# Kernel tuning notes

Hardware: AMD Instinct MI355X
Metric: run time of the kernel (lower is better)

The kernel has to match this reference:

```python
import jax, jax.numpy as jnp
import numpy as np

H, W = 8192, 16384          # dna_shape = (out_features, in_features)
NUM_TRANSFORMS = 8
NUM_POINTS = 1000           # hardcoded in source
CHAOS_ITERS = 10            # hardcoded in source
B = 2048


def setup_inputs() -> dict:
    key = jax.random.key(0)
    k1, k2, k3 = jax.random.split(key, 3)
    x = jax.random.normal(k1, (B, W), dtype=jnp.float32)
    # flat IFS params: [a,b,c,d,e,f,p] per transform; scaled down so affine maps are mostly contractive
    dna_params = jax.random.normal(k2, (NUM_TRANSFORMS * 7,), dtype=jnp.float32) * 0.5
    bias = jax.random.normal(k3, (H,), dtype=jnp.float32)
    return {"x": x, "dna_params": dna_params, "bias": bias}


def reference(x, dna_params, bias):
    params = dna_params.reshape(NUM_TRANSFORMS, 7)  # (T, 7)
    # theta[t] = [[a, b, e], [c, d, f]]  -> (T, 2, 3) affine maps
    theta = jnp.stack([
        jnp.stack([params[:, 0], params[:, 1], params[:, 4]], axis=1),
        jnp.stack([params[:, 2], params[:, 3], params[:, 5]], axis=1),
    ], axis=1)

    key = jax.random.key(1)
    kp, kg = jax.random.split(key)
    points = jax.random.uniform(kp, (NUM_POINTS, 2), dtype=x.dtype) * 2.0 - 1.0  # (N, 2) in [-1, 1)
    logits = jnp.broadcast_to(params[:, 6], (NUM_POINTS, NUM_TRANSFORMS))

    # Chaos game: 10 iterations of hard gumbel-softmax transform selection + affine map
    for i in range(CHAOS_ITERS):
        g = jax.random.gumbel(jax.random.fold_in(kg, i), (NUM_POINTS, NUM_TRANSFORMS), dtype=x.dtype)
        soft = jax.nn.softmax(logits + g, axis=-1)  # tau = 1.0
        hard = jax.nn.one_hot(jnp.argmax(soft, axis=-1), NUM_TRANSFORMS, dtype=soft.dtype)
        gw = hard + soft - jax.lax.stop_gradient(soft)          # straight-through hard sample (N, T)
        t_theta = jnp.einsum('nt,trc->nrc', gw, theta)          # (N, 2, 3) per-point affine
        ph = jnp.concatenate([points, jnp.ones((NUM_POINTS, 1), dtype=points.dtype)], axis=1)  # (N, 3)
        points = jnp.einsum('nrc,nc->nr', t_theta, ph)          # (N, 2)

    # Map attractor points to matrix coordinates
    y_coords = (points[:, 1] + 1.0) * 0.5 * (H - 1)
    x_coords = (points[:, 0] + 1.0) * 0.5 * (W - 1)
    y_low = jnp.clip(jnp.floor(y_coords).astype(jnp.int32), 0, H - 2)
    y_w = y_coords - y_low.astype(y_coords.dtype)
    x_low = jnp.clip(jnp.floor(x_coords).astype(jnp.int32), 0, W - 2)
    x_w = x_coords - x_low.astype(x_coords.dtype)

    # Bilinear gather along in_features: (B, N)
    x_vals = x[:, x_low] * (1.0 - x_w) + x[:, x_low + 1] * x_w

    # Bilinear scatter-add along out_features: (B, H)
    y = jnp.zeros((x.shape[0], H), dtype=x.dtype)
    y = y.at[:, y_low].add(x_vals * (1.0 - y_w))
    y = y.at[:, y_low + 1].add(x_vals * y_w)
    return y / NUM_POINTS + bias
```

## Files before the change

kernel.cpp:

```cpp
#include <hip/hip_runtime.h>
#include <stdint.h>

#ifndef PRNG_PARTITIONABLE
#define PRNG_PARTITIONABLE 1
#endif

namespace {

constexpr int kH  = 8192;
constexpr int kW  = 16384;
constexpr int kNT = 8;
constexpr int kNP = 1000;
constexpr int kCI = 10;

typedef float floatx4 __attribute__((ext_vector_type(4)));

__device__ __forceinline__ uint32_t rotl32(uint32_t x, int n) {
  return (x << n) | (x >> (32 - n));
}

__device__ void threefry2x32(uint32_t k0, uint32_t k1, uint32_t c0, uint32_t c1,
                             uint32_t& o0, uint32_t& o1) {
  const uint32_t ks2 = k0 ^ k1 ^ 0x1BD11BDAu;
  uint32_t x0 = c0 + k0, x1 = c1 + k1;
#define TF_R(r) { x0 += x1; x1 = rotl32(x1, (r)); x1 ^= x0; }
  TF_R(13) TF_R(15) TF_R(26) TF_R(6)
  x0 += k1;  x1 += ks2 + 1u;
  TF_R(17) TF_R(29) TF_R(16) TF_R(24)
  x0 += ks2; x1 += k0 + 2u;
  TF_R(13) TF_R(15) TF_R(26) TF_R(6)
  x0 += k0;  x1 += k1 + 3u;
  TF_R(17) TF_R(29) TF_R(16) TF_R(24)
  x0 += k1;  x1 += ks2 + 4u;
  TF_R(13) TF_R(15) TF_R(26) TF_R(6)
  x0 += ks2; x1 += k0 + 5u;
#undef TF_R
  o0 = x0; o1 = x1;
}

__device__ __forceinline__ uint32_t random_bits32(uint32_t k0, uint32_t k1,
                                                  uint32_t i, uint32_t size) {
#if PRNG_PARTITIONABLE
  uint32_t o0, o1;
  threefry2x32(k0, k1, 0u , i, o0, o1);
  (void)size;
  return o0 ^ o1;
#else
  const uint32_t half = size / 2u;
  const uint32_t j = (i < half) ? i : (i - half);
  uint32_t o0, o1;
  threefry2x32(k0, k1, j, j + half, o0, o1);
  return (i < half) ? o0 : o1;
#endif
}

__device__ __forceinline__ float u01(uint32_t bits) {
  return __uint_as_float((bits >> 9) | 0x3f800000u) - 1.0f;
}

__device__ __forceinline__ int cvt_f32_i32_x86(float v) {
  if (!(v >= -2147483648.0f && v < 2147483648.0f)) return (int)0x80000000;
  return (int)v;
}

__global__ __launch_bounds__(256) void fractal_chaos(
    const float* __restrict__ dna, int4* __restrict__ rec) {
  const int gid  = blockIdx.x * blockDim.x + threadIdx.x;
  const int n    = gid >> 3;
  const int lane = gid & 7;
  if (n >= kNP) return;

  uint32_t kp0, kp1, kg0, kg1;
#if PRNG_PARTITIONABLE
  threefry2x32(0u, 1u, 0u, 0u, kp0, kp1);
  threefry2x32(0u, 1u, 0u, 1u, kg0, kg1);
#else
  uint32_t a0, a1, b0, b1;
  threefry2x32(0u, 1u, 0u, 2u, a0, a1);
  threefry2x32(0u, 1u, 1u, 3u, b0, b1);
  kp0 = a0; kp1 = b0; kg0 = a1; kg1 = b1;
#endif

  const float A  = dna[lane * 7 + 0], Bb = dna[lane * 7 + 1];
  const float C  = dna[lane * 7 + 2], D  = dna[lane * 7 + 3];
  const float E  = dna[lane * 7 + 4], F  = dna[lane * 7 + 5];
  const float P  = dna[lane * 7 + 6];

  float z[kCI];
  #pragma unroll
  for (int i = 0; i < kCI; ++i) {
    uint32_t ki0, ki1;
    threefry2x32(kg0, kg1, 0u, (uint32_t)i, ki0, ki1);
    const uint32_t bb = random_bits32(ki0, ki1, (uint32_t)(n * kNT + lane),
                                      (uint32_t)(kNP * kNT));
    const float u = fmaxf(u01(bb), 1.17549435e-38f);
    const float g = -logf(-logf(u));
    z[i] = P + g;
  }

  const uint32_t bx = random_bits32(kp0, kp1, (uint32_t)(2 * n),     2u * kNP);
  const uint32_t by = random_bits32(kp0, kp1, (uint32_t)(2 * n + 1), 2u * kNP);
  float px = u01(bx) * 2.0f - 1.0f;
  float py = u01(by) * 2.0f - 1.0f;

  #pragma unroll
  for (int i = 0; i < kCI; ++i) {
    float zb = z[i];
    int   bt = lane;
    #pragma unroll
    for (int m = 1; m < 8; m <<= 1) {
      const float zo = __shfl_xor(zb, m, 8);
      const int   to = __shfl_xor(bt, m, 8);
      if (zo > zb || (zo == zb && to < bt)) { zb = zo; bt = to; }
    }
    const float A_ = __shfl(A,  bt, 8), B_ = __shfl(Bb, bt, 8);
    const float C_ = __shfl(C,  bt, 8), D_ = __shfl(D,  bt, 8);
    const float E_ = __shfl(E,  bt, 8), F_ = __shfl(F,  bt, 8);
    const float nx = A_ * px + B_ * py + E_;
    const float ny = C_ * px + D_ * py + F_;
    px = nx; py = ny;
  }

  if (lane == 0) {
    const float xc = ((px + 1.0f) * 0.5f) * (float)(kW - 1);
    const float yc = ((py + 1.0f) * 0.5f) * (float)(kH - 1);
    int xl = cvt_f32_i32_x86(floorf(xc));
    int yl = cvt_f32_i32_x86(floorf(yc));
    xl = min(max(xl, 0), kW - 2);
    yl = min(max(yl, 0), kH - 2);
    const float xw = xc - (float)xl;
    const float yw = yc - (float)yl;
    rec[n] = make_int4(xl, __float_as_int(xw), yl, __float_as_int(yw));
  }
}

__global__ __launch_bounds__(1024) void fractal_apply(
    const float* __restrict__ x, const float* __restrict__ bias,
    const int4* __restrict__ rec, float* __restrict__ out) {
  __shared__ __align__(16) float acc[kH];
  __shared__ __align__(16) float xbuf[kW / 2];

  const int b   = blockIdx.x;
  const int tid = threadIdx.x;

  float4* acc4 = reinterpret_cast<float4*>(acc);
  acc4[tid]        = make_float4(0.f, 0.f, 0.f, 0.f);
  acc4[tid + 1024] = make_float4(0.f, 0.f, 0.f, 0.f);

  const bool havept = tid < kNP;
  int xl = 0, yl = 0;
  float xw = 0.f, yw = 0.f, xw0 = 0.f, w0 = 0.f;
  if (havept) {
    const int4 r = rec[tid];
    xl = r.x; xw = __int_as_float(r.y);
    yl = r.z; yw = __int_as_float(r.w);
    xw0 = 1.0f - xw; w0 = 1.0f - yw;
  }

  const float* __restrict__ xrow = x + (size_t)b * kW;
  float4* xbuf4 = reinterpret_cast<float4*>(xbuf);

  #pragma unroll
  for (int p = 0; p < 2; ++p) {
    const float4* __restrict__ src =
        reinterpret_cast<const float4*>(xrow + p * (kW / 2));
    xbuf4[tid]        = src[tid];
    xbuf4[tid + 1024] = src[tid + 1024];
    __syncthreads();

    if (havept && (xl >> 13) == p) {
      const int loc = xl & (kW / 2 - 1);
      const float v0 = xbuf[loc];
      const float v1 = (loc < kW / 2 - 1) ? xbuf[loc + 1] : xrow[xl + 1];
      const float xv = v0 * xw0 + v1 * xw;
      atomicAdd(&acc[yl],     xv * w0);
      atomicAdd(&acc[yl + 1], xv * yw);
    }
    __syncthreads();
  }

  const float4* __restrict__ bias4 = reinterpret_cast<const float4*>(bias);
  floatx4* __restrict__ out4 =
      reinterpret_cast<floatx4*>(out + (size_t)b * kH);
  #pragma unroll
  for (int i = 0; i < 2; ++i) {
    const int idx = tid + i * 1024;
    const float4 a  = acc4[idx];
    const float4 bi = bias4[idx];
    floatx4 o;
    o.x = a.x / 1000.0f + bi.x;
    o.y = a.y / 1000.0f + bi.y;
    o.z = a.z / 1000.0f + bi.z;
    o.w = a.w / 1000.0f + bi.w;
    __builtin_nontemporal_store(o, &out4[idx]);
  }
}

}

extern "C" void kernel_launch(void* const* d_in, const int* in_sizes, int n_in,
                              void* d_out, int out_size, void* d_ws, size_t ws_size,
                              hipStream_t stream) {
  const float* x    = (const float*)d_in[0];
  const float* dna  = (const float*)d_in[1];
  const float* bias = (const float*)d_in[2];
  float* out = (float*)d_out;
  int4* rec = (int4*)d_ws;

  const int chaosThreads = kNP * 8;
  fractal_chaos<<<(chaosThreads + 255) / 256, 256, 0, stream>>>(dna, rec);

  const int B = in_sizes[0] / kW;
  fractal_apply<<<B, 1024, 0, stream>>>(x, bias, rec, out);
}
```

Before: 50.52 us.

## Replace per-row shared-memory scatter with precomputed CSR gather over output rows

Adds a single-block build kernel that turns the 1000 attractor points into a CSR structure keyed by output row, with pre-scaled weights, an x-sorted point order, and a list of heavily populated rows. The apply kernel no longer stages the whole x row and an 8192-float accumulator in LDS. It gathers only the 1000 needed x values, then computes each output element as a gather-sum over its CSR entries, using wave-level reductions for heavy rows. This removes the large LDS traffic, shared atomics and the 1024-thread blocks. In exchange it adds an extra serial launch and rowptr/entry reads per output element, plus divergence in rows with many entries.

```diff
diff --git a/kernel.cpp b/kernel.cpp
--- a/kernel.cpp
+++ b/kernel.cpp
@@ -12,6 +12,14 @@
 constexpr int kNT = 8;
 constexpr int kNP = 1000;
 constexpr int kCI = 10;
+constexpr int kHeavy = 128;
+constexpr int kMaxHeavy = 32;
+
+constexpr size_t kOffRec    = 0;
+constexpr size_t kOffRowPtr = 16384;
+constexpr size_t kOffEnt    = 49408;
+constexpr size_t kOffOrder  = 65536;
+constexpr size_t kOffHeavy  = 69632;
 
 typedef float floatx4 __attribute__((ext_vector_type(4)));
 
@@ -134,65 +142,178 @@
   }
 }
 
-__global__ __launch_bounds__(1024) void fractal_apply(
+__global__ __launch_bounds__(1024) void fractal_build(
+    const int4* __restrict__ rec, uint32_t* __restrict__ rowptr,
+    uint2* __restrict__ ent, uint32_t* __restrict__ order,
+    uint32_t* __restrict__ heavy ) {
+  __shared__ uint32_t cnt[kH];
+  __shared__ uint32_t seg[1024];
+  __shared__ uint32_t heavyL[kMaxHeavy];
+  __shared__ uint32_t nHeavyL;
+
+  const int t = threadIdx.x;
+  if (t == 0) nHeavyL = 0;
+
+  #pragma unroll
+  for (int i = 0; i < kH / 1024; ++i) cnt[t + i * 1024] = 0;
+  __syncthreads();
+
+  int yl = 0, xl = 0;
+  float w0 = 0.f, w1 = 0.f;
+  const bool hav = t < kNP;
+  if (hav) {
+    const int4 r = rec[t];
+    xl = r.x;
+    yl = r.z;
+    const float yw = __int_as_float(r.w);
+    w0 = (1.0f - yw) * (1.0f / (float)kNP);
+    w1 = yw * (1.0f / (float)kNP);
+    atomicAdd(&cnt[yl], 1u);
+    atomicAdd(&cnt[yl + 1], 1u);
+  }
+  __syncthreads();
+
+  uint32_t s = 0;
+  #pragma unroll
+  for (int i = 0; i < 8; ++i) s += cnt[t * 8 + i];
+  seg[t] = s;
+  __syncthreads();
+  #pragma unroll
+  for (int o = 1; o < 1024; o <<= 1) {
+    uint32_t v = (t >= o) ? seg[t - o] : 0u;
+    __syncthreads();
+    seg[t] += v;
+    __syncthreads();
+  }
+  uint32_t run = (t > 0) ? seg[t - 1] : 0u;
+  const uint32_t total = seg[1023];
+  #pragma unroll
+  for (int i = 0; i < 8; ++i) {
+    const int h = t * 8 + i;
+    const uint32_t c = cnt[h];
+    if (c >= (uint32_t)kHeavy) {
+      const uint32_t p = atomicAdd(&nHeavyL, 1u);
+      if (p < kMaxHeavy) heavyL[p] = (uint32_t)h;
+    }
+    cnt[h] = run;
+    rowptr[h] = run;
+    run += c;
+  }
+  if (t == 1023) rowptr[kH] = total;
+  __syncthreads();
+
+  if (hav) {
+    const uint32_t e0 = atomicAdd(&cnt[yl], 1u);
+    ent[e0] = make_uint2((uint32_t)t, __float_as_uint(w0));
+    const uint32_t e1 = atomicAdd(&cnt[yl + 1], 1u);
+    ent[e1] = make_uint2((uint32_t)t, __float_as_uint(w1));
+  }
+  if (t == 0) heavy[0] = min(nHeavyL, (uint32_t)kMaxHeavy);
+  if (t < kMaxHeavy && t < nHeavyL) heavy[1 + t] = heavyL[t];
+  __syncthreads();
+
+  if (t < 1024) cnt[t] = 0;
+  __syncthreads();
+  const int bx = xl >> 4;
+  if (hav) atomicAdd(&cnt[bx], 1u);
+  __syncthreads();
+  seg[t] = cnt[t];
+  __syncthreads();
+  #pragma unroll
+  for (int o = 1; o < 1024; o <<= 1) {
+    uint32_t v = (t >= o) ? seg[t - o] : 0u;
+    __syncthreads();
+    seg[t] += v;
+    __syncthreads();
+  }
+  cnt[t] = (t > 0) ? seg[t - 1] : 0u;
+  __syncthreads();
+  if (hav) {
+    const uint32_t p = atomicAdd(&cnt[bx], 1u);
+    order[p] = (uint32_t)t;
+  }
+}
+
+__global__ __launch_bounds__(256) void fractal_apply(
     const float* __restrict__ x, const float* __restrict__ bias,
-    const int4* __restrict__ rec, float* __restrict__ out) {
-  __shared__ __align__(16) float acc[kH];
-  __shared__ __align__(16) float xbuf[kW / 2];
-
+    const int4* __restrict__ rec, const uint32_t* __restrict__ rowptr,
+    const uint2* __restrict__ ent, const uint32_t* __restrict__ order,
+    const uint32_t* __restrict__ heavy, float* __restrict__ out) {
+  __shared__ float XV[kNP];
+  __shared__ uint32_t heavyH[kMaxHeavy];
+  __shared__ float heavyS[kMaxHeavy];
+  __shared__ uint32_t nH;
+
+  const int tid = threadIdx.x;
   const int b   = blockIdx.x;
-  const int tid = threadIdx.x;
-
-  float4* acc4 = reinterpret_cast<float4*>(acc);
-  acc4[tid]        = make_float4(0.f, 0.f, 0.f, 0.f);
-  acc4[tid + 1024] = make_float4(0.f, 0.f, 0.f, 0.f);
-
-  const bool havept = tid < kNP;
-  int xl = 0, yl = 0;
-  float xw = 0.f, yw = 0.f, xw0 = 0.f, w0 = 0.f;
-  if (havept) {
-    const int4 r = rec[tid];
-    xl = r.x; xw = __int_as_float(r.y);
-    yl = r.z; yw = __int_as_float(r.w);
-    xw0 = 1.0f - xw; w0 = 1.0f - yw;
-  }
-
   const float* __restrict__ xrow = x + (size_t)b * kW;
-  float4* xbuf4 = reinterpret_cast<float4*>(xbuf);
-
-  #pragma unroll
-  for (int p = 0; p < 2; ++p) {
-    const float4* __restrict__ src =
-        reinterpret_cast<const float4*>(xrow + p * (kW / 2));
-    xbuf4[tid]        = src[tid];
-    xbuf4[tid + 1024] = src[tid + 1024];
-    __syncthreads();
-
-    if (havept && (xl >> 13) == p) {
-      const int loc = xl & (kW / 2 - 1);
-      const float v0 = xbuf[loc];
-      const float v1 = (loc < kW / 2 - 1) ? xbuf[loc + 1] : xrow[xl + 1];
-      const float xv = v0 * xw0 + v1 * xw;
-      atomicAdd(&acc[yl],     xv * w0);
-      atomicAdd(&acc[yl + 1], xv * yw);
-    }
-    __syncthreads();
-  }
-
-  const float4* __restrict__ bias4 = reinterpret_cast<const float4*>(bias);
-  floatx4* __restrict__ out4 =
-      reinterpret_cast<floatx4*>(out + (size_t)b * kH);
-  #pragma unroll
-  for (int i = 0; i < 2; ++i) {
-    const int idx = tid + i * 1024;
-    const float4 a  = acc4[idx];
-    const float4 bi = bias4[idx];
-    floatx4 o;
-    o.x = a.x / 1000.0f + bi.x;
-    o.y = a.y / 1000.0f + bi.y;
-    o.z = a.z / 1000.0f + bi.z;
-    o.w = a.w / 1000.0f + bi.w;
-    __builtin_nontemporal_store(o, &out4[idx]);
+
+  if (tid == 0) nH = heavy[0];
+  if (tid < kMaxHeavy) heavyH[tid] = heavy[1 + tid];
+
+  #pragma unroll
+  for (int j = 0; j < 4; ++j) {
+    const int i = tid + j * 256;
+    if (i < kNP) {
+      const uint32_t n = order[i];
+      const int4 r = rec[n];
+      const int   xl = r.x;
+      const float xw = __int_as_float(r.y);
+      XV[n] = xrow[xl] * (1.0f - xw) + xrow[xl + 1] * xw;
+    }
+  }
+  __syncthreads();
+
+  {
+    const int wid  = tid >> 6;
+    const int lane = tid & 63;
+    const uint32_t nh = nH;
+    for (uint32_t k = wid; k < nh; k += 4) {
+      const uint32_t h = heavyH[k];
+      const uint32_t s = rowptr[h], e = rowptr[h + 1];
+      float p = 0.f;
+      for (uint32_t i = s + lane; i < e; i += 64) {
+        const uint2 en = ent[i];
+        p += XV[en.x] * __uint_as_float(en.y);
+      }
+      #pragma unroll
+      for (int o = 32; o > 0; o >>= 1) p += __shfl_down(p, o);
+      if (lane == 0) heavyS[k] = p;
+    }
+  }
+  __syncthreads();
+
+  const uint32_t nh = nH;
+  const int4* __restrict__ rp4 = reinterpret_cast<const int4*>(rowptr);
+  const floatx4* __restrict__ bias4 = reinterpret_cast<const floatx4*>(bias);
+  floatx4* __restrict__ out4 = reinterpret_cast<floatx4*>(out + (size_t)b * kH);
+
+  #pragma unroll
+  for (int j = 0; j < 8; ++j) {
+    const int g = j * 256 + tid;
+    const int4 rpv = rp4[g];
+    const uint32_t rp_end = rowptr[4 * g + 4];
+    uint32_t rps[5] = {(uint32_t)rpv.x, (uint32_t)rpv.y, (uint32_t)rpv.z,
+                       (uint32_t)rpv.w, rp_end};
+    floatx4 v;
+    #pragma unroll
+    for (int c = 0; c < 4; ++c) {
+      const uint32_t s = rps[c], e = rps[c + 1];
+      float val = 0.f;
+      if (e - s >= (uint32_t)kHeavy) {
+        const uint32_t h = (uint32_t)(4 * g + c);
+        for (uint32_t k = 0; k < nh; ++k)
+          if (heavyH[k] == h) { val = heavyS[k]; break; }
+      } else {
+        for (uint32_t i = s; i < e; ++i) {
+          const uint2 en = ent[i];
+          val += XV[en.x] * __uint_as_float(en.y);
+        }
+      }
+      v[c] = val;
+    }
+    v += bias4[g];
+    __builtin_nontemporal_store(v, &out4[g]);
   }
 }
 
@@ -205,11 +326,18 @@
   const float* dna  = (const float*)d_in[1];
   const float* bias = (const float*)d_in[2];
   float* out = (float*)d_out;
-  int4* rec = (int4*)d_ws;
-
-  const int chaosThreads = kNP * 8;
-  fractal_chaos<<<(chaosThreads + 255) / 256, 256, 0, stream>>>(dna, rec);
+
+  char* ws = (char*)d_ws;
+  int4*     rec    = (int4*)(ws + kOffRec);
+  uint32_t* rowptr = (uint32_t*)(ws + kOffRowPtr);
+  uint2*    ent    = (uint2*)(ws + kOffEnt);
+  uint32_t* order  = (uint32_t*)(ws + kOffOrder);
+  uint32_t* heavy  = (uint32_t*)(ws + kOffHeavy);
+
+  fractal_chaos<<<(kNP * 8 + 255) / 256, 256, 0, stream>>>(dna, rec);
+  fractal_build<<<1, 1024, 0, stream>>>(rec, rowptr, ent, order, heavy);
 
   const int B = in_sizes[0] / kW;
-  fractal_apply<<<B, 1024, 0, stream>>>(x, bias, rec, out);
-}
+  fractal_apply<<<B, 256, 0, stream>>>(x, bias, rec, rowptr, ent, order,
+                                       heavy, out);
+}
```

New measurement: 72.28 us. +43.1%, slower.

## Compact touched output rows and gather x directly instead of staging full rows

Applied to the files above, without the earlier changes.

Adds a single-block build kernel that marks which output columns are hit by the attractor points, builds a bitmap, a prefix-sum compaction of those columns, and per-point compact indices. The apply kernel now reads only the two x values each point needs straight from global memory rather than staging the whole 64 KB row in shared memory. It writes bias directly for untouched columns and accumulates into a small compact shared buffer for touched ones. This cuts global read traffic and shared memory per block, at the cost of an extra serial kernel launch, scattered scalar stores for partially touched vectors, and uncoalesced gathers.

```diff
diff --git a/kernel.cpp b/kernel.cpp
--- a/kernel.cpp
+++ b/kernel.cpp
@@ -12,6 +12,13 @@
 constexpr int kNT = 8;
 constexpr int kNP = 1000;
 constexpr int kCI = 10;
+constexpr int kU  = 2048;
+
+constexpr size_t kOffRec    = 0;
+constexpr size_t kOffRec2   = 16384;
+constexpr size_t kOffBins   = 32768;
+constexpr size_t kOffBitmap = 40960;
+constexpr size_t kOffHdr    = 41984;
 
 typedef float floatx4 __attribute__((ext_vector_type(4)));
 
@@ -134,65 +141,136 @@
   }
 }
 
-__global__ __launch_bounds__(1024) void fractal_apply(
+__global__ __launch_bounds__(1024) void fractal_build(
+    const int4* __restrict__ rec, int4* __restrict__ rec2,
+    uint32_t* __restrict__ bins, uint32_t* __restrict__ bitmap,
+    uint32_t* __restrict__ hdr) {
+  __shared__ uint32_t mark[kH];
+  __shared__ uint32_t seg[1024];
+
+  const int t = threadIdx.x;
+
+  #pragma unroll
+  for (int i = 0; i < kH / 1024; ++i) mark[t + i * 1024] = 0u;
+  __syncthreads();
+
+  int xl = 0, yl = 0;
+  uint32_t xwb = 0, ywb = 0;
+  const bool hav = t < kNP;
+  if (hav) {
+    const int4 r = rec[t];
+    xl = r.x; xwb = (uint32_t)r.y;
+    yl = r.z; ywb = (uint32_t)r.w;
+    mark[yl] = 1u;
+    mark[yl + 1] = 1u;
+  }
+  __syncthreads();
+
+  if (t < kH / 32) {
+    uint32_t w = 0;
+    #pragma unroll
+    for (int j = 0; j < 32; ++j) w |= mark[t * 32 + j] << j;
+    bitmap[t] = w;
+  }
+
+  uint32_t s = 0;
+  #pragma unroll
+  for (int i = 0; i < 8; ++i) s += mark[t * 8 + i];
+  seg[t] = s;
+  __syncthreads();
+  #pragma unroll
+  for (int o = 1; o < 1024; o <<= 1) {
+    uint32_t v = (t >= o) ? seg[t - o] : 0u;
+    __syncthreads();
+    seg[t] += v;
+    __syncthreads();
+  }
+  uint32_t run = (t > 0) ? seg[t - 1] : 0u;
+  if (t == 1023) hdr[0] = seg[1023];
+  #pragma unroll
+  for (int i = 0; i < 8; ++i) {
+    const int h = t * 8 + i;
+    const uint32_t m = mark[h];
+    if (m) bins[run] = (uint32_t)h;
+    mark[h] = run;
+    run += m;
+  }
+  __syncthreads();
+
+  if (hav) {
+    const uint32_t c0 = mark[yl];
+    const uint32_t c1 = mark[yl + 1];
+    rec2[t] = make_int4(xl, (int)xwb, (int)(c0 | (c1 << 16)), (int)ywb);
+  }
+}
+
+__global__ __launch_bounds__(256) void fractal_apply(
     const float* __restrict__ x, const float* __restrict__ bias,
-    const int4* __restrict__ rec, float* __restrict__ out) {
-  __shared__ __align__(16) float acc[kH];
-  __shared__ __align__(16) float xbuf[kW / 2];
-
+    const int4* __restrict__ rec2, const uint32_t* __restrict__ bins,
+    const uint32_t* __restrict__ bitmap, const uint32_t* __restrict__ hdr,
+    float* __restrict__ out) {
+  __shared__ float acc[kU];
+  __shared__ uint32_t bmw[kH / 32];
+
+  const int tid = threadIdx.x;
   const int b   = blockIdx.x;
-  const int tid = threadIdx.x;
+  const float* __restrict__ xrow = x + (size_t)b * kW;
+  float* __restrict__ outrow = out + (size_t)b * kH;
 
   float4* acc4 = reinterpret_cast<float4*>(acc);
-  acc4[tid]        = make_float4(0.f, 0.f, 0.f, 0.f);
-  acc4[tid + 1024] = make_float4(0.f, 0.f, 0.f, 0.f);
-
-  const bool havept = tid < kNP;
-  int xl = 0, yl = 0;
-  float xw = 0.f, yw = 0.f, xw0 = 0.f, w0 = 0.f;
-  if (havept) {
-    const int4 r = rec[tid];
-    xl = r.x; xw = __int_as_float(r.y);
-    yl = r.z; yw = __int_as_float(r.w);
-    xw0 = 1.0f - xw; w0 = 1.0f - yw;
-  }
-
-  const float* __restrict__ xrow = x + (size_t)b * kW;
-  float4* xbuf4 = reinterpret_cast<float4*>(xbuf);
-
-  #pragma unroll
-  for (int p = 0; p < 2; ++p) {
-    const float4* __restrict__ src =
-        reinterpret_cast<const float4*>(xrow + p * (kW / 2));
-    xbuf4[tid]        = src[tid];
-    xbuf4[tid + 1024] = src[tid + 1024];
-    __syncthreads();
-
-    if (havept && (xl >> 13) == p) {
-      const int loc = xl & (kW / 2 - 1);
-      const float v0 = xbuf[loc];
-      const float v1 = (loc < kW / 2 - 1) ? xbuf[loc + 1] : xrow[xl + 1];
-      const float xv = v0 * xw0 + v1 * xw;
-      atomicAdd(&acc[yl],     xv * w0);
-      atomicAdd(&acc[yl + 1], xv * yw);
-    }
-    __syncthreads();
-  }
-
-  const float4* __restrict__ bias4 = reinterpret_cast<const float4*>(bias);
-  floatx4* __restrict__ out4 =
-      reinterpret_cast<floatx4*>(out + (size_t)b * kH);
-  #pragma unroll
-  for (int i = 0; i < 2; ++i) {
-    const int idx = tid + i * 1024;
-    const float4 a  = acc4[idx];
-    const float4 bi = bias4[idx];
-    floatx4 o;
-    o.x = a.x / 1000.0f + bi.x;
-    o.y = a.y / 1000.0f + bi.y;
-    o.z = a.z / 1000.0f + bi.z;
-    o.w = a.w / 1000.0f + bi.w;
-    __builtin_nontemporal_store(o, &out4[idx]);
+  acc4[tid]       = make_float4(0.f, 0.f, 0.f, 0.f);
+  acc4[tid + 256] = make_float4(0.f, 0.f, 0.f, 0.f);
+  bmw[tid] = bitmap[tid];
+  const uint32_t U = hdr[0];
+  __syncthreads();
+
+  int4  r[4];
+  float v0[4], v1[4];
+  #pragma unroll
+  for (int j = 0; j < 4; ++j) {
+    const int n = tid + j * 256;
+    if (n < kNP) {
+      r[j] = rec2[n];
+      v0[j] = xrow[r[j].x];
+      v1[j] = xrow[r[j].x + 1];
+    }
+  }
+
+  const floatx4* __restrict__ bias4 = reinterpret_cast<const floatx4*>(bias);
+  floatx4* __restrict__ outrow4 = reinterpret_cast<floatx4*>(outrow);
+  #pragma unroll
+  for (int j = 0; j < 8; ++j) {
+    const int g = j * 256 + tid;
+    const floatx4 bv = bias4[g];
+    const uint32_t nib = (bmw[g >> 3] >> ((g & 7) * 4)) & 0xFu;
+    if (nib == 0) {
+      __builtin_nontemporal_store(bv, &outrow4[g]);
+    } else {
+      float* o = outrow + 4 * g;
+      if (!(nib & 1u)) o[0] = bv.x;
+      if (!(nib & 2u)) o[1] = bv.y;
+      if (!(nib & 4u)) o[2] = bv.z;
+      if (!(nib & 8u)) o[3] = bv.w;
+    }
+  }
+
+  #pragma unroll
+  for (int j = 0; j < 4; ++j) {
+    const int n = tid + j * 256;
+    if (n < kNP) {
+      const float xw = __int_as_float(r[j].y);
+      const float yw = __int_as_float(r[j].w);
+      const uint32_t c01 = (uint32_t)r[j].z;
+      const float xv = v0[j] * (1.0f - xw) + v1[j] * xw;
+      atomicAdd(&acc[c01 & 0xFFFFu], xv * (1.0f - yw));
+      atomicAdd(&acc[c01 >> 16],     xv * yw);
+    }
+  }
+  __syncthreads();
+
+  for (uint32_t i = tid; i < U; i += 256) {
+    const uint32_t c = bins[i];
+    outrow[c] = acc[i] / 1000.0f + bias[c];
   }
 }
 
@@ -205,11 +283,17 @@
   const float* dna  = (const float*)d_in[1];
   const float* bias = (const float*)d_in[2];
   float* out = (float*)d_out;
-  int4* rec = (int4*)d_ws;
-
-  const int chaosThreads = kNP * 8;
-  fractal_chaos<<<(chaosThreads + 255) / 256, 256, 0, stream>>>(dna, rec);
+
+  char* ws = (char*)d_ws;
+  int4*     rec    = (int4*)(ws + kOffRec);
+  int4*     rec2   = (int4*)(ws + kOffRec2);
+  uint32_t* bins   = (uint32_t*)(ws + kOffBins);
+  uint32_t* bitmap = (uint32_t*)(ws + kOffBitmap);
+  uint32_t* hdr    = (uint32_t*)(ws + kOffHdr);
+
+  fractal_chaos<<<(kNP * 8 + 255) / 256, 256, 0, stream>>>(dna, rec);
+  fractal_build<<<1, 1024, 0, stream>>>(rec, rec2, bins, bitmap, hdr);
 
   const int B = in_sizes[0] / kW;
-  fractal_apply<<<B, 1024, 0, stream>>>(x, bias, rec, out);
-}
+  fractal_apply<<<B, 256, 0, stream>>>(x, bias, rec2, bins, bitmap, hdr, out);
+}
```

New measurement: 80.76 us. +59.8%, slower.

## Gather x values directly per point and process several rows per block

Applied to the files above, without the earlier changes.

Instead of staging each full 64 KB x row through shared memory, each point-thread now loads only its two needed x values straight from global memory, prefetching the next row while the current one is scattered. Each block handles four batch rows, reusing the loaded point records and re-zeroing the LDS accumulator between rows. Barriers become a custom waitcnt-plus-s_barrier sequence. This cuts x read traffic to only the touched elements and reduces block launch and setup overhead. In exchange, global loads become scattered and there are fewer, longer-lived blocks.

```diff
diff --git a/kernel.cpp b/kernel.cpp
--- a/kernel.cpp
+++ b/kernel.cpp
@@ -12,8 +12,11 @@
 constexpr int kNT = 8;
 constexpr int kNP = 1000;
 constexpr int kCI = 10;
+constexpr int kRPB = 4;
 
 typedef float floatx4 __attribute__((ext_vector_type(4)));
+
+#define BAR_LDS() asm volatile("s_waitcnt lgkmcnt(0)\n\ts_barrier" ::: "memory")
 
 __device__ __forceinline__ uint32_t rotl32(uint32_t x, int n) {
   return (x << n) | (x >> (32 - n));
@@ -136,63 +139,75 @@
 
 __global__ __launch_bounds__(1024) void fractal_apply(
     const float* __restrict__ x, const float* __restrict__ bias,
-    const int4* __restrict__ rec, float* __restrict__ out) {
+    const int4* __restrict__ rec, float* __restrict__ out, int B) {
   __shared__ __align__(16) float acc[kH];
-  __shared__ __align__(16) float xbuf[kW / 2];
-
-  const int b   = blockIdx.x;
   const int tid = threadIdx.x;
+  const int r0  = blockIdx.x * kRPB;
+
+  const bool hav = tid < kNP;
+  int xl = 0, yl = 0;
+  float xw = 0.f, yw = 0.f;
+  if (hav) {
+    const int4 rr = rec[tid];
+    xl = rr.x; xw = __int_as_float(rr.y);
+    yl = rr.z; yw = __int_as_float(rr.w);
+  }
+  const float xw0 = 1.0f - xw;
+  const float w0  = 1.0f - yw;
 
   float4* acc4 = reinterpret_cast<float4*>(acc);
   acc4[tid]        = make_float4(0.f, 0.f, 0.f, 0.f);
   acc4[tid + 1024] = make_float4(0.f, 0.f, 0.f, 0.f);
 
-  const bool havept = tid < kNP;
-  int xl = 0, yl = 0;
-  float xw = 0.f, yw = 0.f, xw0 = 0.f, w0 = 0.f;
-  if (havept) {
-    const int4 r = rec[tid];
-    xl = r.x; xw = __int_as_float(r.y);
-    yl = r.z; yw = __int_as_float(r.w);
-    xw0 = 1.0f - xw; w0 = 1.0f - yw;
-  }
-
-  const float* __restrict__ xrow = x + (size_t)b * kW;
-  float4* xbuf4 = reinterpret_cast<float4*>(xbuf);
+  float v0 = 0.f, v1 = 0.f;
+  if (hav && r0 < B) {
+    const float* xp = x + (size_t)r0 * kW + xl;
+    v0 = xp[0];
+    v1 = xp[1];
+  }
+
+  BAR_LDS();
+
+  const floatx4* __restrict__ bias4 = reinterpret_cast<const floatx4*>(bias);
 
   #pragma unroll
-  for (int p = 0; p < 2; ++p) {
-    const float4* __restrict__ src =
-        reinterpret_cast<const float4*>(xrow + p * (kW / 2));
-    xbuf4[tid]        = src[tid];
-    xbuf4[tid + 1024] = src[tid + 1024];
-    __syncthreads();
-
-    if (havept && (xl >> 13) == p) {
-      const int loc = xl & (kW / 2 - 1);
-      const float v0 = xbuf[loc];
-      const float v1 = (loc < kW / 2 - 1) ? xbuf[loc + 1] : xrow[xl + 1];
+  for (int it = 0; it < kRPB; ++it) {
+    const int r = r0 + it;
+    if (r >= B) break;
+
+    if (hav) {
       const float xv = v0 * xw0 + v1 * xw;
       atomicAdd(&acc[yl],     xv * w0);
       atomicAdd(&acc[yl + 1], xv * yw);
     }
-    __syncthreads();
-  }
-
-  const float4* __restrict__ bias4 = reinterpret_cast<const float4*>(bias);
-  floatx4* __restrict__ out4 =
-      reinterpret_cast<floatx4*>(out + (size_t)b * kH);
-  #pragma unroll
-  for (int i = 0; i < 2; ++i) {
-    const int idx = tid + i * 1024;
-    const float4 a  = acc4[idx];
-    const float4 bi = bias4[idx];
-    floatx4 o;
-    o.x = a.x / 1000.0f + bi.x;
-    o.y = a.y / 1000.0f + bi.y;
-    o.z = a.z / 1000.0f + bi.z;
-    o.w = a.w / 1000.0f + bi.w;
-    __builtin_nontemporal_store(o, &out4[idx]);
+
+    if (hav && it + 1 < kRPB && r + 1 < B) {
+      const float* xp = x + (size_t)(r + 1) * kW + xl;
+      v0 = xp[0];
+      v1 = xp[1];
+    }
+
+    BAR_LDS();
+
+    float* __restrict__ outrow = out + (size_t)r * kH;
+    floatx4* __restrict__ out4 = reinterpret_cast<floatx4*>(outrow);
+    #pragma unroll
+    for (int j = 0; j < 2; ++j) {
+      const int g = tid + j * 1024;
+      const float4 a  = acc4[g];
+      const floatx4 bi = bias4[g];
+      floatx4 o;
+      o.x = a.x / 1000.0f + bi.x;
+      o.y = a.y / 1000.0f + bi.y;
+      o.z = a.z / 1000.0f + bi.z;
+      o.w = a.w / 1000.0f + bi.w;
+      __builtin_nontemporal_store(o, &out4[g]);
+      acc4[g] = make_float4(0.f, 0.f, 0.f, 0.f);
+    }
+
+    if (it + 1 < kRPB && r + 1 < B) {
+      BAR_LDS();
+    }
   }
 }
 
@@ -207,9 +222,9 @@
   float* out = (float*)d_out;
   int4* rec = (int4*)d_ws;
 
-  const int chaosThreads = kNP * 8;
-  fractal_chaos<<<(chaosThreads + 255) / 256, 256, 0, stream>>>(dna, rec);
+  fractal_chaos<<<(kNP * 8 + 255) / 256, 256, 0, stream>>>(dna, rec);
 
   const int B = in_sizes[0] / kW;
-  fractal_apply<<<B, 1024, 0, stream>>>(x, bias, rec, out);
-}
+  fractal_apply<<<(B + kRPB - 1) / kRPB, 1024, 0, stream>>>(x, bias, rec,
+                                                            out, B);
+}
```

New measurement: 42.28 us. 16.3% less time.
